# Performance work log

Measured on AMD Instinct MI355X. Metric: run time of the kernel, lower is better.

The kernel has to match this reference:

```python
import jax, jax.numpy as jnp
import numpy as np

D = 1024
HEADS = 16
HEAD_DIM = D // HEADS
B = 4
L = 1024


def setup_inputs() -> dict:
    key = jax.random.key(0)
    kq, kk, kv, kw, kb = jax.random.split(key, 5)
    Q = jax.random.normal(kq, (B, L, D), dtype=jnp.float32)
    K = jax.random.normal(kk, (B, L, D), dtype=jnp.float32)
    V = jax.random.normal(kv, (B, L, D), dtype=jnp.float32)
    # Output projection H: torch nn.Linear(D, D) -> weight (D, D), bias (D,)
    lim = 1.0 / np.sqrt(D)
    W_H = jax.random.uniform(kw, (D, D), minval=-lim, maxval=lim, dtype=jnp.float32)
    b_H = jax.random.uniform(kb, (D,), minval=-lim, maxval=lim, dtype=jnp.float32)
    mask = 0  # falsy -> no masking branch, matching `if mask` in the source
    return {"Q": Q, "K": K, "V": V, "W_H": W_H, "b_H": b_H, "mask": mask}


def reference(Q, K, V, W_H, b_H, mask):
    batch, q_len, _ = Q.shape
    k_len = K.shape[1]
    Qh = Q.reshape(batch, q_len, HEADS, HEAD_DIM)
    Kh = K.reshape(batch, k_len, HEADS, HEAD_DIM)
    Vh = V.reshape(batch, k_len, HEADS, HEAD_DIM)
    scores = jnp.einsum('bqhd,bkhd->bhqk', Qh, Kh)  # [B,H,Lq,Lk]
    if mask:  # mask is a Python scalar (0 -> skip), as in source
        scores = jnp.where(mask == 0, -jnp.inf, scores)
    # NOTE: source scales by sqrt(D), not sqrt(head_dim)
    attn = jax.nn.softmax(scores / np.sqrt(D).astype(np.float32), axis=3)
    out = jnp.einsum('bhql,blhd->bqhd', attn, Vh).reshape(batch, q_len, D)
    return out @ W_H.T + b_H
```

## Files before the change

### kernel.cpp

```cpp
#include <hip/hip_runtime.h>
#include <hip/hip_bf16.h>

typedef __attribute__((ext_vector_type(4))) float f32x4;
typedef __attribute__((ext_vector_type(8))) short bf16x8;

constexpr int Bn  = 4;
constexpr int Ln  = 1024;
constexpr int Dn  = 1024;
constexpr int Hn  = 16;
constexpr int HDn = 64;

static __device__ __forceinline__ unsigned short bf16r(float f) {
    union { float f; unsigned int u; } x;
    x.f = f;
    unsigned int r = x.u + 0x7fffu + ((x.u >> 16) & 1u);
    return (unsigned short)(r >> 16);
}

static __device__ __forceinline__ unsigned int pk2(float a, float b) {
    return (unsigned int)bf16r(a) | ((unsigned int)bf16r(b) << 16);
}

__global__ __launch_bounds__(256) void prep_kernel(
    const float* __restrict__ Kg, const float* __restrict__ Vg,
    const float* __restrict__ Wg, unsigned short* __restrict__ Kbf,
    unsigned short* __restrict__ Vtg, unsigned short* __restrict__ Wbf)
{
    const int tid = threadIdx.x;
    if (blockIdx.z == 4) {
        const int r0 = blockIdx.x * 64, c0 = blockIdx.y * 64;
#pragma unroll 4
        for (int i = 0; i < 4; ++i) {
            int e4 = i * 256 + tid;
            int r = e4 >> 4, c4 = e4 & 15;
            const float* p = Wg + (size_t)(r0 + r) * Dn + c0 + c4 * 4;
            float4 v = *(const float4*)p;
            ushort4 o;
            o.x = bf16r(v.x); o.y = bf16r(v.y); o.z = bf16r(v.z); o.w = bf16r(v.w);
            *(ushort4*)(Wbf + (size_t)(r0 + r) * Dn + c0 + c4 * 4) = o;
        }
        return;
    }

    __shared__ unsigned short T[64][72];
    const int k0 = blockIdx.x * 64;
    const int h  = blockIdx.y;
    const int b  = blockIdx.z;
    const float* Kb = Kg + (size_t)b * Ln * Dn + h * HDn;
    const float* Vb = Vg + (size_t)b * Ln * Dn + h * HDn;
    unsigned short* Ko = Kbf + (size_t)b * Ln * Dn + h * HDn;

#pragma unroll 4
    for (int i = 0; i < 4; ++i) {
        int e4 = i * 256 + tid;
        int r = e4 >> 4, c4 = e4 & 15;
        float4 kv = *(const float4*)(Kb + (size_t)(k0 + r) * Dn + c4 * 4);
        ushort4 o;
        o.x = bf16r(kv.x); o.y = bf16r(kv.y); o.z = bf16r(kv.z); o.w = bf16r(kv.w);
        *(ushort4*)(Ko + (size_t)(k0 + r) * Dn + c4 * 4) = o;
        float4 vv = *(const float4*)(Vb + (size_t)(k0 + r) * Dn + c4 * 4);
        T[c4 * 4 + 0][r] = bf16r(vv.x);
        T[c4 * 4 + 1][r] = bf16r(vv.y);
        T[c4 * 4 + 2][r] = bf16r(vv.z);
        T[c4 * 4 + 3][r] = bf16r(vv.w);
    }
    __syncthreads();
    unsigned short* out = Vtg + ((size_t)(b * Hn + h) * HDn) * Ln + k0;
#pragma unroll 2
    for (int i = 0; i < 2; ++i) {
        int e8 = i * 256 + tid;
        int r = e8 >> 3, c8 = e8 & 7;
        *(uint4*)(out + (size_t)r * Ln + c8 * 8) = *(const uint4*)&T[r][c8 * 8];
    }
}

__global__ __launch_bounds__(512) void attn_kernel(
    const float* __restrict__ Qg, const unsigned short* __restrict__ Kbf,
    const unsigned short* __restrict__ Vtg, unsigned short* __restrict__ Xg)
{
    __shared__ uint4 Ks4[64][9];
    __shared__ uint4 Vts4[64][9];
    __shared__ uint2 Ps2[256][18];

    const int tid  = threadIdx.x;
    const int wave = tid >> 6;
    const int lane = tid & 63;
    const int l16  = lane & 15;
    const int quad = lane >> 4;
    const int wb   = wave * 32;

    const int flat = blockIdx.x;
    const int xcd  = flat & 7;
    const int j    = flat >> 3;
    const int qt   = j & 3;
    const int gg   = j >> 2;
    const int g    = xcd + 8 * gg;
    const int h    = g & 15;
    const int b    = g >> 4;
    const int q0   = qt * 256;

    const uint4* Kb4  = (const uint4*)(Kbf + (size_t)b * Ln * Dn + h * HDn);
    const uint4* Vtb4 = (const uint4*)(Vtg + ((size_t)(b * Hn + h) * HDn) * Ln);

    bf16x8 bq[2][2];
#pragma unroll 2
    for (int hf = 0; hf < 2; ++hf) {
        const float* qp = Qg + ((size_t)b * Ln + q0 + wb + hf * 16 + l16) * Dn
                             + h * HDn + quad * 8;
        float4 a0 = *(const float4*)qp;
        float4 a1 = *(const float4*)(qp + 4);
        float4 a2 = *(const float4*)(qp + 32);
        float4 a3 = *(const float4*)(qp + 36);
        bq[hf][0][0] = (short)bf16r(a0.x); bq[hf][0][1] = (short)bf16r(a0.y);
        bq[hf][0][2] = (short)bf16r(a0.z); bq[hf][0][3] = (short)bf16r(a0.w);
        bq[hf][0][4] = (short)bf16r(a1.x); bq[hf][0][5] = (short)bf16r(a1.y);
        bq[hf][0][6] = (short)bf16r(a1.z); bq[hf][0][7] = (short)bf16r(a1.w);
        bq[hf][1][0] = (short)bf16r(a2.x); bq[hf][1][1] = (short)bf16r(a2.y);
        bq[hf][1][2] = (short)bf16r(a2.z); bq[hf][1][3] = (short)bf16r(a2.w);
        bq[hf][1][4] = (short)bf16r(a3.x); bq[hf][1][5] = (short)bf16r(a3.y);
        bq[hf][1][6] = (short)bf16r(a3.z); bq[hf][1][7] = (short)bf16r(a3.w);
    }

    const float SC = 1.4426950408889634f / 32.0f;

    float lsum[2] = {0.f, 0.f};
    f32x4 Oacc[2][4];
#pragma unroll 2
    for (int hf = 0; hf < 2; ++hf)
#pragma unroll 4
        for (int d = 0; d < 4; ++d) Oacc[hf][d] = (f32x4){0.f, 0.f, 0.f, 0.f};

    const int sr = tid >> 3, sc = tid & 7;
    uint4 kreg, vreg;
    {
        kreg = Kb4[(size_t)sr * 128 + sc];
        vreg = Vtb4[(size_t)sr * 128 + sc];
    }

    for (int it = 0; it < Ln / 64; ++it) {
        __syncthreads();
        Ks4[sr][sc]  = kreg;
        Vts4[sr][sc] = vreg;
        if (it + 1 < Ln / 64) {
            kreg = Kb4[(size_t)(((it + 1) * 64) + sr) * 128 + sc];
            vreg = Vtb4[(size_t)sr * 128 + (it + 1) * 8 + sc];
        }
        __syncthreads();

        f32x4 st[2][4];
        __builtin_amdgcn_s_setprio(1);
#pragma unroll 4
        for (int n = 0; n < 4; ++n) {
            bf16x8 a0 = *(const bf16x8*)&Ks4[n * 16 + l16][quad];
            bf16x8 a1 = *(const bf16x8*)&Ks4[n * 16 + l16][4 + quad];
#pragma unroll 2
            for (int hf = 0; hf < 2; ++hf) {
                f32x4 acc = (f32x4){0.f, 0.f, 0.f, 0.f};
                acc = __builtin_amdgcn_mfma_f32_16x16x32_bf16(a0, bq[hf][0], acc, 0, 0, 0);
                acc = __builtin_amdgcn_mfma_f32_16x16x32_bf16(a1, bq[hf][1], acc, 0, 0, 0);
                st[hf][n] = acc;
            }
        }
        __builtin_amdgcn_s_setprio(0);

#pragma unroll 2
        for (int hf = 0; hf < 2; ++hf) {
            float ls = 0.f;
#pragma unroll 4
            for (int n = 0; n < 4; ++n) {
                float p0 = __builtin_amdgcn_exp2f(st[hf][n][0] * SC);
                float p1 = __builtin_amdgcn_exp2f(st[hf][n][1] * SC);
                float p2 = __builtin_amdgcn_exp2f(st[hf][n][2] * SC);
                float p3 = __builtin_amdgcn_exp2f(st[hf][n][3] * SC);
                ls += (p0 + p1) + (p2 + p3);
                uint2 w;
                w.x = pk2(p0, p1);
                w.y = pk2(p2, p3);
                Ps2[wb + hf * 16 + l16][n * 4 + quad] = w;
            }
            lsum[hf] += ls;
        }

        __builtin_amdgcn_s_setprio(1);
#pragma unroll 2
        for (int kk = 0; kk < 2; ++kk) {
            bf16x8 bv[4];
#pragma unroll 4
            for (int dt = 0; dt < 4; ++dt)
                bv[dt] = *(const bf16x8*)&Vts4[dt * 16 + l16][kk * 4 + quad];
#pragma unroll 2
            for (int hf = 0; hf < 2; ++hf) {
                bf16x8 ap = *(const bf16x8*)&Ps2[wb + hf * 16 + l16][kk * 8 + quad * 2];
#pragma unroll 4
                for (int dt = 0; dt < 4; ++dt)
                    Oacc[hf][dt] = __builtin_amdgcn_mfma_f32_16x16x32_bf16(
                        ap, bv[dt], Oacc[hf][dt], 0, 0, 0);
            }
        }
        __builtin_amdgcn_s_setprio(0);
    }

    float inv[2];
#pragma unroll 2
    for (int hf = 0; hf < 2; ++hf) {
        float rs = lsum[hf];
        rs += __shfl_xor(rs, 16, 64);
        rs += __shfl_xor(rs, 32, 64);
        inv[hf] = __builtin_amdgcn_rcpf(rs);
    }

    unsigned short* Xb = Xg + ((size_t)b * Ln + q0 + wb) * Dn + h * HDn;
#pragma unroll 2
    for (int hf = 0; hf < 2; ++hf)
#pragma unroll 4
        for (int r = 0; r < 4; ++r) {
            float iv = __shfl(inv[hf], quad * 4 + r, 64);
            int row = hf * 16 + quad * 4 + r;
#pragma unroll 4
            for (int dt = 0; dt < 4; ++dt)
                Xb[(size_t)row * Dn + dt * 16 + l16] = bf16r(Oacc[hf][dt][r] * iv);
        }
}

__global__ __launch_bounds__(256) void proj_kernel(
    const unsigned short* __restrict__ Xg, const unsigned short* __restrict__ Wbf,
    const float* __restrict__ bg, float* __restrict__ Yg)
{
    __shared__ unsigned short XsL[128 * 64];
    __shared__ unsigned short WsL[64 * 64];

    const int tid  = threadIdx.x;
    const int wave = tid >> 6;
    const int lane = tid & 63;
    const int l16  = lane & 15;
    const int quad = lane >> 4;
    const int mw   = (wave & 1) * 64;
    const int nw   = (wave >> 1) * 32;

    const int m0 = blockIdx.x * 128;
    const int n0 = blockIdx.y * 64;

    f32x4 acc[4][2];
#pragma unroll 4
    for (int mt = 0; mt < 4; ++mt)
#pragma unroll 2
        for (int nt = 0; nt < 2; ++nt)
            acc[mt][nt] = (f32x4){0.f, 0.f, 0.f, 0.f};

    for (int it = 0; it < Dn / 64; ++it) {
        const int kk0 = it * 64;
        __syncthreads();
#pragma unroll 4
        for (int i = 0; i < 4; ++i) {
            int fl = i * 256 + tid;
            int r = fl >> 3, c8 = fl & 7;
            __builtin_amdgcn_global_load_lds(
                (const __attribute__((address_space(1))) void*)
                    (Xg + (size_t)(m0 + r) * Dn + kk0 + c8 * 8),
                (__attribute__((address_space(3))) void*)&XsL[fl * 8],
                16, 0, 0);
        }
#pragma unroll 2
        for (int i = 0; i < 2; ++i) {
            int fl = i * 256 + tid;
            int r = fl >> 3, c8 = fl & 7;
            __builtin_amdgcn_global_load_lds(
                (const __attribute__((address_space(1))) void*)
                    (Wbf + (size_t)(n0 + r) * Dn + kk0 + c8 * 8),
                (__attribute__((address_space(3))) void*)&WsL[fl * 8],
                16, 0, 0);
        }
        __syncthreads();

        __builtin_amdgcn_s_setprio(1);
#pragma unroll 2
        for (int ks = 0; ks < 2; ++ks) {
            bf16x8 af[4], bfr[2];
#pragma unroll 4
            for (int mt = 0; mt < 4; ++mt)
                af[mt] = *(const bf16x8*)&XsL[(mw + mt * 16 + l16) * 64 + ks * 32 + quad * 8];
#pragma unroll 2
            for (int nt = 0; nt < 2; ++nt)
                bfr[nt] = *(const bf16x8*)&WsL[(nw + nt * 16 + l16) * 64 + ks * 32 + quad * 8];
#pragma unroll 4
            for (int mt = 0; mt < 4; ++mt)
#pragma unroll 2
                for (int nt = 0; nt < 2; ++nt)
                    acc[mt][nt] = __builtin_amdgcn_mfma_f32_16x16x32_bf16(
                        af[mt], bfr[nt], acc[mt][nt], 0, 0, 0);
        }
        __builtin_amdgcn_s_setprio(0);
    }

#pragma unroll 2
    for (int nt = 0; nt < 2; ++nt) {
        int col = n0 + nw + nt * 16 + l16;
        float bb = bg[col];
#pragma unroll 4
        for (int mt = 0; mt < 4; ++mt)
#pragma unroll 4
            for (int r = 0; r < 4; ++r) {
                int row = m0 + mw + mt * 16 + quad * 4 + r;
                Yg[(size_t)row * Dn + col] = acc[mt][nt][r] + bb;
            }
    }
}

extern "C" void kernel_launch(void* const* d_in, const int* in_sizes, int n_in,
                              void* d_out, int out_size, void* d_ws, size_t ws_size,
                              hipStream_t stream) {
    const float* Q    = (const float*)d_in[0];
    const float* K    = (const float*)d_in[1];
    const float* V    = (const float*)d_in[2];
    const float* W    = (const float*)d_in[3];
    const float* bias = (const float*)d_in[4];

    unsigned short* Kbf = (unsigned short*)d_ws;
    unsigned short* Vt  = Kbf + (size_t)Bn * Ln * Dn;
    unsigned short* Wbf = Vt  + (size_t)Bn * Ln * Dn;
    unsigned short* X   = Wbf + (size_t)Dn * Dn;
    float* Y = (float*)d_out;

    dim3 gp(Ln / 64, Hn, Bn + 1);
    prep_kernel<<<gp, 256, 0, stream>>>(K, V, W, Kbf, Vt, Wbf);

    attn_kernel<<<dim3(256, 1, 1), 512, 0, stream>>>(Q, Kbf, Vt, X);

    dim3 g2(Bn * Ln / 128, Dn / 64);
    proj_kernel<<<g2, 256, 0, stream>>>(X, Wbf, bias, Y);
}
```

Before: 151.2 us.

## Double-buffer K/V LDS tiles and replace padding with XOR swizzle

The attention loop now keeps two LDS buffers for K and V^T tiles. It writes the next tile after compute and uses a single barrier per iteration instead of two, with register prefetch running two tiles ahead. The padded LDS layouts (stride 9/18) are replaced by unpadded arrays with XOR-swizzled column indices to avoid bank conflicts. This doubles the K/V LDS footprint, which could affect occupancy.

```diff
diff --git a/kernel.cpp b/kernel.cpp
--- a/kernel.cpp
+++ b/kernel.cpp
@@ -78,15 +78,16 @@
     const float* __restrict__ Qg, const unsigned short* __restrict__ Kbf,
     const unsigned short* __restrict__ Vtg, unsigned short* __restrict__ Xg)
 {
-    __shared__ uint4 Ks4[64][9];
-    __shared__ uint4 Vts4[64][9];
-    __shared__ uint2 Ps2[256][18];
+    __shared__ uint4 Ks4[2][64][8];
+    __shared__ uint4 Vts4[2][64][8];
+    __shared__ uint2 Ps2[256][16];
 
     const int tid  = threadIdx.x;
     const int wave = tid >> 6;
     const int lane = tid & 63;
     const int l16  = lane & 15;
     const int quad = lane >> 4;
+    const int r7   = l16 & 7;
     const int wb   = wave * 32;
 
     const int flat = blockIdx.x;
@@ -131,28 +132,27 @@
         for (int d = 0; d < 4; ++d) Oacc[hf][d] = (f32x4){0.f, 0.f, 0.f, 0.f};
 
     const int sr = tid >> 3, sc = tid & 7;
+    const int scs = sc ^ (sr & 7);
     uint4 kreg, vreg;
-    {
-        kreg = Kb4[(size_t)sr * 128 + sc];
-        vreg = Vtb4[(size_t)sr * 128 + sc];
-    }
-
-    for (int it = 0; it < Ln / 64; ++it) {
-        __syncthreads();
-        Ks4[sr][sc]  = kreg;
-        Vts4[sr][sc] = vreg;
-        if (it + 1 < Ln / 64) {
-            kreg = Kb4[(size_t)(((it + 1) * 64) + sr) * 128 + sc];
-            vreg = Vtb4[(size_t)sr * 128 + (it + 1) * 8 + sc];
-        }
-        __syncthreads();
+
+    kreg = Kb4[(size_t)sr * 128 + sc];
+    vreg = Vtb4[(size_t)sr * 128 + sc];
+    Ks4[0][sr][scs]  = kreg;
+    Vts4[0][sr][scs] = vreg;
+    kreg = Kb4[(size_t)(64 + sr) * 128 + sc];
+    vreg = Vtb4[(size_t)sr * 128 + 8 + sc];
+    __syncthreads();
+
+    constexpr int NT = Ln / 64;
+    for (int it = 0; it < NT; ++it) {
+        const int cur = it & 1;
 
         f32x4 st[2][4];
         __builtin_amdgcn_s_setprio(1);
 #pragma unroll 4
         for (int n = 0; n < 4; ++n) {
-            bf16x8 a0 = *(const bf16x8*)&Ks4[n * 16 + l16][quad];
-            bf16x8 a1 = *(const bf16x8*)&Ks4[n * 16 + l16][4 + quad];
+            bf16x8 a0 = __builtin_bit_cast(bf16x8, Ks4[cur][n * 16 + l16][quad ^ r7]);
+            bf16x8 a1 = __builtin_bit_cast(bf16x8, Ks4[cur][n * 16 + l16][(4 + quad) ^ r7]);
 #pragma unroll 2
             for (int hf = 0; hf < 2; ++hf) {
                 f32x4 acc = (f32x4){0.f, 0.f, 0.f, 0.f};
@@ -176,7 +176,7 @@
                 uint2 w;
                 w.x = pk2(p0, p1);
                 w.y = pk2(p2, p3);
-                Ps2[wb + hf * 16 + l16][n * 4 + quad] = w;
+                Ps2[wb + hf * 16 + l16][(n * 4 + quad) ^ (r7 << 1)] = w;
             }
             lsum[hf] += ls;
         }
@@ -187,10 +187,12 @@
             bf16x8 bv[4];
 #pragma unroll 4
             for (int dt = 0; dt < 4; ++dt)
-                bv[dt] = *(const bf16x8*)&Vts4[dt * 16 + l16][kk * 4 + quad];
+                bv[dt] = __builtin_bit_cast(bf16x8,
+                    Vts4[cur][dt * 16 + l16][(kk * 4 + quad) ^ r7]);
 #pragma unroll 2
             for (int hf = 0; hf < 2; ++hf) {
-                bf16x8 ap = *(const bf16x8*)&Ps2[wb + hf * 16 + l16][kk * 8 + quad * 2];
+                int blk = (kk * 4 + quad) ^ r7;
+                bf16x8 ap = *(const bf16x8*)&Ps2[wb + hf * 16 + l16][blk * 2];
 #pragma unroll 4
                 for (int dt = 0; dt < 4; ++dt)
                     Oacc[hf][dt] = __builtin_amdgcn_mfma_f32_16x16x32_bf16(
@@ -198,6 +200,16 @@
             }
         }
         __builtin_amdgcn_s_setprio(0);
+
+        if (it + 1 < NT) {
+            Ks4[cur ^ 1][sr][scs]  = kreg;
+            Vts4[cur ^ 1][sr][scs] = vreg;
+            if (it + 2 < NT) {
+                kreg = Kb4[(size_t)((it + 2) * 64 + sr) * 128 + sc];
+                vreg = Vtb4[(size_t)sr * 128 + (it + 2) * 8 + sc];
+            }
+        }
+        __syncthreads();
     }
 
     float inv[2];
```

Result: faster. 147.5 us (-2.5%).
